# Kernel tuning notes

Measured on AMD Instinct MI355X. Metric: run time of the kernel, lower is better.

## Reference

```python
import jax, jax.numpy as jnp
import numpy as np

B, N, DIM = 2, 2048, 512
HEADS, DIM_HEAD = 8, 64
INNER = HEADS * DIM_HEAD  # 512
SCALE = DIM_HEAD ** -0.5


def setup_inputs() -> dict:
    key = jax.random.key(0)
    k1, k2, k3, k4, k5 = jax.random.split(key, 5)
    s = 0.02
    return {
        "x1": jax.random.normal(k1, (B, N, DIM), jnp.float32),
        "x2": jax.random.normal(k2, (B, N, DIM), jnp.float32),
        "W_qk": jax.random.normal(k3, (DIM, 2 * INNER), jnp.float32) * s,
        "W_v": jax.random.normal(k4, (DIM, INNER), jnp.float32) * s,
        "W_out": jax.random.normal(k5, (INNER, DIM), jnp.float32) * s,
        "b_out": jnp.zeros((DIM,), jnp.float32),
    }


def _split_heads(t):
    # [b, n, h*d] -> [b, h, n, d]
    b, n, _ = t.shape
    return t.reshape(b, n, HEADS, DIM_HEAD).transpose(0, 2, 1, 3)


def reference(x1, x2, W_qk, W_v, W_out, b_out):
    # to_qk(x1) -> chunk into k, v ; to_v(x2) -> q  (names in orig are swapped)
    kv = x1 @ W_qk                      # [b, n1, 2*inner]
    k, v = jnp.split(kv, 2, axis=-1)
    q = x2 @ W_v                        # [b, n2, inner]
    q, k, v = _split_heads(q), _split_heads(k), _split_heads(v)  # [b,h,n,d]
    dots = jnp.einsum("bhid,bhjd->bhij", q, k) * SCALE  # [b,h,n2,n1]
    attn = jax.nn.softmax(dots, axis=-1)
    out = jnp.einsum("bhij,bhjd->bhid", attn, v)         # [b,h,n2,d]
    out = out.transpose(0, 2, 1, 3).reshape(out.shape[0], out.shape[2], INNER)
    return out @ W_out + b_out          # [b, n2, dim]
```

## Files before the change

kernel.cpp:

```cpp
#include <hip/hip_runtime.h>

typedef short bf16x8 __attribute__((ext_vector_type(8)));
typedef short bf16x4 __attribute__((ext_vector_type(4)));
typedef float f32x4 __attribute__((ext_vector_type(4)));
typedef float f32x16 __attribute__((ext_vector_type(16)));
typedef unsigned short u16;
typedef unsigned int u32;
typedef u16 u16x8 __attribute__((ext_vector_type(8)));
typedef u16 u16x4 __attribute__((ext_vector_type(4)));

#define DEV __device__ __forceinline__

DEV u16 f2bf(float f) {
  unsigned u = __float_as_uint(f);
  u += 0x7fff + ((u >> 16) & 1);
  return (u16)(u >> 16);
}

DEV int cvtpk(float lo, float hi) {
  int r;
  asm("v_cvt_pk_bf16_f32 %0, %1, %2" : "=v"(r) : "v"(lo), "v"(hi));
  return r;
}

DEV int pkbf(float lo, float hi) {
  return __builtin_amdgcn_perm(__float_as_uint(hi) + 0x8000u,
                               __float_as_uint(lo) + 0x8000u, 0x07060302u);
}

#define MFMA16(a, b, c) __builtin_amdgcn_mfma_f32_16x16x32_bf16(a, b, c, 0, 0, 0)
#define MFMA3216(a, b, c) __builtin_amdgcn_mfma_f32_32x32x16_bf16(a, b, c, 0, 0, 0)

#if __has_builtin(__builtin_amdgcn_mfma_f32_32x32x8bf16_1k)
#define HAVE_PV8 1
#define PVMFMA(a, b, c) __builtin_amdgcn_mfma_f32_32x32x8bf16_1k(a, b, c, 0, 0, 0)
#else
#define HAVE_PV8 0
#endif

#if __has_builtin(__builtin_amdgcn_exp2f)
#define QSCALE 0.18033688011112042f
#define EXPFN(x) __builtin_amdgcn_exp2f(x)
#else
#define QSCALE 0.125f
#define EXPFN(x) __expf(x)
#endif

#define GLD16(gp, lp)                                                     \
  __builtin_amdgcn_global_load_lds(                                       \
      (const __attribute__((address_space(1))) u32*)(gp),                 \
      (__attribute__((address_space(3))) u32*)(lp), 16, 0, 0)

__global__ __launch_bounds__(256) void wprep(
    const float* __restrict__ Wqk, const float* __restrict__ Wv,
    const float* __restrict__ Wout,
    const float* __restrict__ x1, const float* __restrict__ x2,
    u16* __restrict__ WqkT, u16* __restrict__ WvT, u16* __restrict__ WoutT,
    u16* __restrict__ x1b, u16* __restrict__ x2b) {
  __shared__ float tf[32][33];
  int bx = blockIdx.x, t = threadIdx.x;
  if (bx >= 1024) {
    int id = bx - 1024;
    const float* src = id < 1024 ? x1 : x2;
    u16* dst = id < 1024 ? x1b : x2b;
    long base = (long)(id & 1023) * 2048 + t * 8;
    float4 f0 = *(const float4*)(src + base);
    float4 f1 = *(const float4*)(src + base + 4);
    u16x8 o;
    o[0] = f2bf(f0.x); o[1] = f2bf(f0.y); o[2] = f2bf(f0.z); o[3] = f2bf(f0.w);
    o[4] = f2bf(f1.x); o[5] = f2bf(f1.y); o[6] = f2bf(f1.z); o[7] = f2bf(f1.w);
    *(u16x8*)(dst + base) = o;
    return;
  }
  const float* src; u16* dst; int Ncols; int id;
  if (bx < 512)      { id = bx;       src = Wqk;  dst = WqkT;  Ncols = 1024; }
  else if (bx < 768) { id = bx - 512; src = Wv;   dst = WvT;   Ncols = 512; }
  else               { id = bx - 768; src = Wout; dst = WoutT; Ncols = 512; }
  int tilesPerRow = Ncols >> 5;
  int tr = id / tilesPerRow, tc = id % tilesPerRow;
  int r0 = tr * 32, c0 = tc * 32;
  {
    int r = t >> 3, c4 = (t & 7) * 4;
    float4 v = *(const float4*)(src + (long)(r0 + r) * Ncols + c0 + c4);
    tf[r][c4] = v.x; tf[r][c4 + 1] = v.y; tf[r][c4 + 2] = v.z; tf[r][c4 + 3] = v.w;
  }
  __syncthreads();
  {
    int c = t >> 3, r4 = (t & 7) * 4;
    u16x4 o;
    o[0] = f2bf(tf[r4][c]); o[1] = f2bf(tf[r4 + 1][c]);
    o[2] = f2bf(tf[r4 + 2][c]); o[3] = f2bf(tf[r4 + 3][c]);
    *(u16x4*)(dst + (long)(c0 + c) * 512 + r0 + r4) = o;
  }
}

__global__ __launch_bounds__(256) void qkv_gemm(
    const u16* __restrict__ x1b, const u16* __restrict__ x2b,
    const u16* __restrict__ WqkT, const u16* __restrict__ WvT,
    u16* __restrict__ out_q, u16* __restrict__ out_k, u16* __restrict__ out_vt) {
  __shared__ u16 sA[2][128 * 40];
  __shared__ u16 sB[2][64 * 40];
  int bx = blockIdx.x, t = threadIdx.x;
  bool isQ = bx < 256;
  int bx2 = isQ ? bx : bx - 256;
  const u16* Ap = isQ ? x2b : x1b;
  const u16* BT = isQ ? WvT : WqkT;
  int m0 = (bx2 & 31) * 128, n0 = (bx2 >> 5) * 64;
  int w = t >> 6, l = t & 63, lm = l & 15, lq = l >> 4;

  f32x4 zero = {0.f, 0.f, 0.f, 0.f};
  f32x4 acc[2][4];
#pragma unroll
  for (int i = 0; i < 2; ++i)
#pragma unroll
    for (int j = 0; j < 4; ++j) acc[i][j] = zero;

  int sm = t >> 2;
  int skc = (t & 3) * 8;
  const u16* gA = Ap + (long)(m0 + sm) * 512 + skc;
  const u16* gB = BT + (long)(n0 + sm) * 512 + skc;

  bf16x8 a0 = *(const bf16x8*)(gA);
  bf16x8 a1 = *(const bf16x8*)(gA + 64 * 512);
  bf16x8 b0 = *(const bf16x8*)(gB);
  *(bf16x8*)(sA[0] + sm * 40 + skc) = a0;
  *(bf16x8*)(sA[0] + (sm + 64) * 40 + skc) = a1;
  *(bf16x8*)(sB[0] + sm * 40 + skc) = b0;
  __syncthreads();

  for (int kt = 0; kt < 16; ++kt) {
    int cur = kt & 1;
    if (kt < 15) {
      a0 = *(const bf16x8*)(gA + (kt + 1) * 32);
      a1 = *(const bf16x8*)(gA + 64 * 512 + (kt + 1) * 32);
      b0 = *(const bf16x8*)(gB + (kt + 1) * 32);
    }
    bf16x8 af[2], bfr[4];
    af[0] = *(const bf16x8*)(sA[cur] + (w * 32 + lm) * 40 + lq * 8);
    af[1] = *(const bf16x8*)(sA[cur] + (w * 32 + 16 + lm) * 40 + lq * 8);
#pragma unroll
    for (int s = 0; s < 4; ++s)
      bfr[s] = *(const bf16x8*)(sB[cur] + (s * 16 + lm) * 40 + lq * 8);
#pragma unroll
    for (int ms = 0; ms < 2; ++ms)
#pragma unroll
      for (int s = 0; s < 4; ++s)
        acc[ms][s] = MFMA16(af[ms], bfr[s], acc[ms][s]);
    if (kt < 15) {
      int nxt = 1 - cur;
      *(bf16x8*)(sA[nxt] + sm * 40 + skc) = a0;
      *(bf16x8*)(sA[nxt] + (sm + 64) * 40 + skc) = a1;
      *(bf16x8*)(sB[nxt] + sm * 40 + skc) = b0;
    }
    __syncthreads();
  }

#pragma unroll
  for (int ms = 0; ms < 2; ++ms) {
    int gmBase = m0 + w * 32 + ms * 16 + lq * 4;
#pragma unroll
    for (int s = 0; s < 4; ++s) {
      int gc = n0 + s * 16 + lm;
      int b = gmBase >> 11, n = gmBase & 2047;
      if (isQ) {
#pragma unroll
        for (int r = 0; r < 4; ++r)
          out_q[(((long)(b << 3) + (gc >> 6)) * 2048 + n + r) * 64 + (gc & 63)] =
              f2bf(acc[ms][s][r] * QSCALE);
      } else if (gc < 512) {
#pragma unroll
        for (int r = 0; r < 4; ++r)
          out_k[(((long)(b << 3) + (gc >> 6)) * 2048 + n + r) * 64 + (gc & 63)] =
              f2bf(acc[ms][s][r]);
      } else {
        int c = gc - 512, h = c >> 6, d = c & 63;
        u16x4 vv;
#pragma unroll
        for (int r = 0; r < 4; ++r) vv[r] = f2bf(acc[ms][s][r]);
        *(u16x4*)(out_vt + (((long)(b << 3) + h) * 64 + d) * 2048 + n) = vv;
      }
    }
  }
}

__global__ __launch_bounds__(256, 2) void attn(
    const u16* __restrict__ Q, const u16* __restrict__ K,
    const u16* __restrict__ Vt, u16* __restrict__ O) {
  int id = blockIdx.x;
  int bh = id & 15, qt = id >> 4;
  int b = bh >> 3, h = bh & 7;
  const u16* Kh = K + (long)bh * 2048 * 64;
  const u16* Vh = Vt + (long)bh * 64 * 2048;
  int t = threadIdx.x, w = t >> 6, lane = t & 63, ln = lane & 31, hi = lane >> 5;
  int g = w & 1, kh = w >> 1;

  __shared__ u16 smem[2][2][2][4096];

  bf16x8 qf[4];
  {
    const u16* qp = Q + (long)bh * 2048 * 64 + (long)(qt * 64 + g * 32 + ln) * 64 + hi * 8;
#pragma unroll
    for (int dc = 0; dc < 4; ++dc) qf[dc] = *(const bf16x8*)(qp + dc * 16);
  }

  f32x16 accO[2];
#pragma unroll
  for (int dt = 0; dt < 2; ++dt)
#pragma unroll
    for (int i = 0; i < 16; ++i) accO[dt][i] = 0.f;
  float dacc = 0.f;

  f32x16 fz;
#pragma unroll
  for (int i = 0; i < 16; ++i) fz[i] = 0.f;

  int lrow = lane >> 3;
  int swz = ((lane & 7) ^ lrow) * 8;
  const u16* gKl = Kh + (long)(kh * 1024 + g * 32 + lrow) * 64 + swz;
  const u16* gVl = Vh + (long)(g * 32 + lrow) * 2048 + kh * 1024 + swz;

  auto stage = [&](int jt, int buf) {
    u16* sK = smem[buf][0][kh];
    u16* sV = smem[buf][1][kh];
    const u16* gk = gKl + (long)jt * 4096;
    const u16* gv = gVl + jt * 64;
#pragma unroll
    for (int i = 0; i < 4; ++i) {
      GLD16(gk + i * 512, sK + (g * 32 + i * 8) * 64);
      GLD16(gv + (long)i * 16384, sV + (g * 32 + i * 8) * 64);
    }
  };

  stage(0, 0);
  __syncthreads();

  int swl = ln & 7;
  for (int jt = 0; jt < 16; ++jt) {
    int cur = jt & 1;
    if (jt < 15) stage(jt + 1, cur ^ 1);
    const u16* sKh = smem[cur][0][kh];
    const u16* sVh = smem[cur][1][kh];
#pragma unroll
    for (int kt2 = 0; kt2 < 2; ++kt2) {
      int rowK = (kt2 * 32 + ln) * 64;
      bf16x8 kf0 = *(const bf16x8*)(sKh + rowK + ((0 * 2 + hi) ^ swl) * 8);
      bf16x8 kf1 = *(const bf16x8*)(sKh + rowK + ((1 * 2 + hi) ^ swl) * 8);
      bf16x8 kf2 = *(const bf16x8*)(sKh + rowK + ((2 * 2 + hi) ^ swl) * 8);
      bf16x8 kf3 = *(const bf16x8*)(sKh + rowK + ((3 * 2 + hi) ^ swl) * 8);
      __builtin_amdgcn_s_setprio(1);
      f32x16 st = MFMA3216(kf0, qf[0], fz);
      st = MFMA3216(kf1, qf[1], st);
      st = MFMA3216(kf2, qf[2], st);
      st = MFMA3216(kf3, qf[3], st);
      __builtin_amdgcn_s_setprio(0);
      float p[16];
#pragma unroll
      for (int i = 0; i < 16; ++i) p[i] = EXPFN(st[i]);
      float q0 = (p[0] + p[1]) + (p[2] + p[3]);
      float q1 = (p[4] + p[5]) + (p[6] + p[7]);
      float q2 = (p[8] + p[9]) + (p[10] + p[11]);
      float q3 = (p[12] + p[13]) + (p[14] + p[15]);
      dacc += (q0 + q1) + (q2 + q3);
#if HAVE_PV8
      __builtin_amdgcn_s_setprio(1);
#pragma unroll
      for (int c = 0; c < 4; ++c) {
        union { int2 i2; bf16x4 v; } u;
        u.i2.x = cvtpk(p[c * 4 + 0], p[c * 4 + 1]);
        u.i2.y = cvtpk(p[c * 4 + 2], p[c * 4 + 3]);
#pragma unroll
        for (int dt = 0; dt < 2; ++dt) {
          bf16x4 vf = *(const bf16x4*)(sVh + (dt * 32 + ln) * 64 +
                                       (((kt2 * 4 + c) ^ swl) * 8) + hi * 4);
          accO[dt] = PVMFMA(vf, u.v, accO[dt]);
        }
      }
      __builtin_amdgcn_s_setprio(0);
#else
      __builtin_amdgcn_s_setprio(1);
#pragma unroll
      for (int c2 = 0; c2 < 2; ++c2) {
        int o0x = pkbf(p[c2 * 8 + 0], p[c2 * 8 + 1]);
        int o0y = pkbf(p[c2 * 8 + 2], p[c2 * 8 + 3]);
        int o1x = pkbf(p[c2 * 8 + 4], p[c2 * 8 + 5]);
        int o1y = pkbf(p[c2 * 8 + 6], p[c2 * 8 + 7]);
        int s0x = __shfl_xor(o0x, 32), s0y = __shfl_xor(o0y, 32);
        int s1x = __shfl_xor(o1x, 32), s1y = __shfl_xor(o1y, 32);
        union { int4 i4; bf16x8 v; } u;
        if (hi) { u.i4.x = s1x; u.i4.y = s1y; u.i4.z = o1x; u.i4.w = o1y; }
        else    { u.i4.x = o0x; u.i4.y = o0y; u.i4.z = s0x; u.i4.w = s0y; }
#pragma unroll
        for (int dt = 0; dt < 2; ++dt) {
          bf16x8 vf = *(const bf16x8*)(sVh + (dt * 32 + ln) * 64 +
                                       (((kt2 * 4 + c2 * 2 + hi) ^ swl) * 8));
          accO[dt] = MFMA3216(vf, u.v, accO[dt]);
        }
      }
      __builtin_amdgcn_s_setprio(0);
#endif
    }
    __syncthreads();
  }

  float* cb = (float*)&smem[0][0][0][0];
  float* base = cb + g * 2112;
  if (kh == 1) {
#pragma unroll
    for (int dt = 0; dt < 2; ++dt)
#pragma unroll
      for (int i = 0; i < 16; ++i)
        base[(dt * 16 + i) * 64 + hi * 32 + ln] = accO[dt][i];
    base[2048 + hi * 32 + ln] = dacc;
  }
  __syncthreads();
  if (kh == 0) {
#pragma unroll
    for (int dt = 0; dt < 2; ++dt)
#pragma unroll
      for (int i = 0; i < 16; ++i)
        accO[dt][i] += base[(dt * 16 + i) * 64 + hi * 32 + ln];
    dacc += base[2048 + hi * 32 + ln];
    dacc += __shfl_xor(dacc, 32);
    float inv = 1.f / dacc;

    u16* Ob = O + ((long)b * 2048 + qt * 64 + g * 32 + ln) * 512 + h * 64;
#pragma unroll
    for (int dt = 0; dt < 2; ++dt)
#pragma unroll
      for (int gq = 0; gq < 4; ++gq) {
        u16x4 o;
#pragma unroll
        for (int rr = 0; rr < 4; ++rr) o[rr] = f2bf(accO[dt][gq * 4 + rr] * inv);
        *(u16x4*)(Ob + dt * 32 + gq * 8 + hi * 4) = o;
      }
  }
}

__global__ __launch_bounds__(128) void out_gemm(
    const u16* __restrict__ A, const u16* __restrict__ BT,
    float* __restrict__ out_f, const float* __restrict__ bias) {
  __shared__ u16 sA[2][64 * 40];
  __shared__ u16 sB[2][32 * 40];
  int t = threadIdx.x, bx = blockIdx.x;
  int m0 = (bx & 63) * 64, n0 = (bx >> 6) * 32;
  int w = t >> 6, l = t & 63, lm = l & 15, lq = l >> 4;

  f32x4 zero = {0.f, 0.f, 0.f, 0.f};
  f32x4 acc[2][2];
#pragma unroll
  for (int i = 0; i < 2; ++i)
#pragma unroll
    for (int j = 0; j < 2; ++j) acc[i][j] = zero;

  int ar = t >> 1, akc = (t & 1) * 16;
  int br = t >> 2, bkc = (t & 3) * 8;
  const u16* gA = A + (long)(m0 + ar) * 512 + akc;
  const u16* gB = BT + (long)(n0 + br) * 512 + bkc;

  bf16x8 a0 = *(const bf16x8*)(gA);
  bf16x8 a1 = *(const bf16x8*)(gA + 8);
  bf16x8 b0 = *(const bf16x8*)(gB);
  *(bf16x8*)(sA[0] + ar * 40 + akc) = a0;
  *(bf16x8*)(sA[0] + ar * 40 + akc + 8) = a1;
  *(bf16x8*)(sB[0] + br * 40 + bkc) = b0;
  __syncthreads();

  for (int kt = 0; kt < 16; ++kt) {
    int cur = kt & 1;
    if (kt < 15) {
      a0 = *(const bf16x8*)(gA + (kt + 1) * 32);
      a1 = *(const bf16x8*)(gA + (kt + 1) * 32 + 8);
      b0 = *(const bf16x8*)(gB + (kt + 1) * 32);
    }
    bf16x8 af[2], bfr[2];
    af[0] = *(const bf16x8*)(sA[cur] + (w * 32 + lm) * 40 + lq * 8);
    af[1] = *(const bf16x8*)(sA[cur] + (w * 32 + 16 + lm) * 40 + lq * 8);
    bfr[0] = *(const bf16x8*)(sB[cur] + (lm)*40 + lq * 8);
    bfr[1] = *(const bf16x8*)(sB[cur] + (16 + lm) * 40 + lq * 8);
#pragma unroll
    for (int ms = 0; ms < 2; ++ms)
#pragma unroll
      for (int s = 0; s < 2; ++s)
        acc[ms][s] = MFMA16(af[ms], bfr[s], acc[ms][s]);
    if (kt < 15) {
      int nxt = 1 - cur;
      *(bf16x8*)(sA[nxt] + ar * 40 + akc) = a0;
      *(bf16x8*)(sA[nxt] + ar * 40 + akc + 8) = a1;
      *(bf16x8*)(sB[nxt] + br * 40 + bkc) = b0;
    }
    __syncthreads();
  }

#pragma unroll
  for (int ms = 0; ms < 2; ++ms) {
    int gmBase = m0 + w * 32 + ms * 16 + lq * 4;
#pragma unroll
    for (int s = 0; s < 2; ++s) {
      int gc = n0 + s * 16 + lm;
      float bv = bias[gc];
#pragma unroll
      for (int r = 0; r < 4; ++r)
        out_f[(long)(gmBase + r) * 512 + gc] = acc[ms][s][r] + bv;
    }
  }
}

extern "C" void kernel_launch(void* const* d_in, const int* in_sizes, int n_in,
                              void* d_out, int out_size, void* d_ws, size_t ws_size,
                              hipStream_t stream) {
  const float* x1 = (const float*)d_in[0];
  const float* x2 = (const float*)d_in[1];
  const float* Wqk = (const float*)d_in[2];
  const float* Wv = (const float*)d_in[3];
  const float* Wout = (const float*)d_in[4];
  const float* bout = (const float*)d_in[5];
  float* out = (float*)d_out;

  u16* ws = (u16*)d_ws;
  const long SZ = 2097152;
  u16* Qw = ws;
  u16* Kw = ws + SZ;
  u16* Vtw = ws + 2 * SZ;
  u16* Ow = ws + 3 * SZ;
  u16* WqkT = ws + 4 * SZ;
  u16* WvT = WqkT + 524288;
  u16* WoutT = WvT + 262144;
  u16* x1b = WoutT + 262144;
  u16* x2b = x1b + SZ;

  wprep<<<3072, 256, 0, stream>>>(Wqk, Wv, Wout, x1, x2, WqkT, WvT, WoutT, x1b, x2b);
  qkv_gemm<<<768, 256, 0, stream>>>(x1b, x2b, WqkT, WvT, Qw, Kw, Vtw);
  attn<<<512, 256, 0, stream>>>(Qw, Kw, Vtw, Ow);
  out_gemm<<<1024, 128, 0, stream>>>(Ow, WoutT, out, bout);
}
```

Before: 127.4 us.

## Fuse fp32-to-bf16 activation conversion into QKV GEMM via direct-to-LDS loads

Drops the separate pass that converted x1/x2 to bf16 in the prep kernel. The QKV GEMM now streams fp32 activations straight into an XOR-swizzled LDS tile with global_load_lds and converts them to bf16 on the fly with packed cvt instructions before the MFMA. This removes a full write and re-read of the bf16 activation copies and shrinks the prep launch. In exchange the GEMM reads twice the bytes per A tile and spends extra ALU work converting values, and A-tile LDS use doubles.

```diff
diff --git a/kernel.cpp b/kernel.cpp
--- a/kernel.cpp
+++ b/kernel.cpp
@@ -54,24 +54,9 @@
 __global__ __launch_bounds__(256) void wprep(
     const float* __restrict__ Wqk, const float* __restrict__ Wv,
     const float* __restrict__ Wout,
-    const float* __restrict__ x1, const float* __restrict__ x2,
-    u16* __restrict__ WqkT, u16* __restrict__ WvT, u16* __restrict__ WoutT,
-    u16* __restrict__ x1b, u16* __restrict__ x2b) {
+    u16* __restrict__ WqkT, u16* __restrict__ WvT, u16* __restrict__ WoutT) {
   __shared__ float tf[32][33];
   int bx = blockIdx.x, t = threadIdx.x;
-  if (bx >= 1024) {
-    int id = bx - 1024;
-    const float* src = id < 1024 ? x1 : x2;
-    u16* dst = id < 1024 ? x1b : x2b;
-    long base = (long)(id & 1023) * 2048 + t * 8;
-    float4 f0 = *(const float4*)(src + base);
-    float4 f1 = *(const float4*)(src + base + 4);
-    u16x8 o;
-    o[0] = f2bf(f0.x); o[1] = f2bf(f0.y); o[2] = f2bf(f0.z); o[3] = f2bf(f0.w);
-    o[4] = f2bf(f1.x); o[5] = f2bf(f1.y); o[6] = f2bf(f1.z); o[7] = f2bf(f1.w);
-    *(u16x8*)(dst + base) = o;
-    return;
-  }
   const float* src; u16* dst; int Ncols; int id;
   if (bx < 512)      { id = bx;       src = Wqk;  dst = WqkT;  Ncols = 1024; }
   else if (bx < 768) { id = bx - 512; src = Wv;   dst = WvT;   Ncols = 512; }
@@ -95,15 +80,15 @@
 }
 
 __global__ __launch_bounds__(256) void qkv_gemm(
-    const u16* __restrict__ x1b, const u16* __restrict__ x2b,
+    const float* __restrict__ x1, const float* __restrict__ x2,
     const u16* __restrict__ WqkT, const u16* __restrict__ WvT,
     u16* __restrict__ out_q, u16* __restrict__ out_k, u16* __restrict__ out_vt) {
-  __shared__ u16 sA[2][128 * 40];
-  __shared__ u16 sB[2][64 * 40];
+  __shared__ __align__(16) float sA32[2][128 * 32];
+  __shared__ __align__(16) u16 sB[2][64 * 40];
   int bx = blockIdx.x, t = threadIdx.x;
   bool isQ = bx < 256;
   int bx2 = isQ ? bx : bx - 256;
-  const u16* Ap = isQ ? x2b : x1b;
+  const float* Ap = isQ ? x2 : x1;
   const u16* BT = isQ ? WvT : WqkT;
   int m0 = (bx2 & 31) * 128, n0 = (bx2 >> 5) * 64;
   int w = t >> 6, l = t & 63, lm = l & 15, lq = l >> 4;
@@ -115,29 +100,45 @@
 #pragma unroll
     for (int j = 0; j < 4; ++j) acc[i][j] = zero;
 
+  int dr = l >> 3;
+  int dc = (l & 7) ^ dr;
+  const float* gAsrc = Ap + (long)(m0 + w * 32 + dr) * 512 + dc * 4;
+
+  auto stageA = [&](int kt, int buf) {
+#pragma unroll
+    for (int i = 0; i < 4; ++i)
+      GLD16(gAsrc + kt * 32 + i * 8 * 512, sA32[buf] + (w * 32 + i * 8) * 32);
+  };
+
   int sm = t >> 2;
   int skc = (t & 3) * 8;
-  const u16* gA = Ap + (long)(m0 + sm) * 512 + skc;
   const u16* gB = BT + (long)(n0 + sm) * 512 + skc;
 
-  bf16x8 a0 = *(const bf16x8*)(gA);
-  bf16x8 a1 = *(const bf16x8*)(gA + 64 * 512);
+  stageA(0, 0);
   bf16x8 b0 = *(const bf16x8*)(gB);
-  *(bf16x8*)(sA[0] + sm * 40 + skc) = a0;
-  *(bf16x8*)(sA[0] + (sm + 64) * 40 + skc) = a1;
   *(bf16x8*)(sB[0] + sm * 40 + skc) = b0;
   __syncthreads();
 
+  int sw7 = lm & 7;
   for (int kt = 0; kt < 16; ++kt) {
     int cur = kt & 1;
     if (kt < 15) {
-      a0 = *(const bf16x8*)(gA + (kt + 1) * 32);
-      a1 = *(const bf16x8*)(gA + 64 * 512 + (kt + 1) * 32);
+      stageA(kt + 1, cur ^ 1);
       b0 = *(const bf16x8*)(gB + (kt + 1) * 32);
     }
     bf16x8 af[2], bfr[4];
-    af[0] = *(const bf16x8*)(sA[cur] + (w * 32 + lm) * 40 + lq * 8);
-    af[1] = *(const bf16x8*)(sA[cur] + (w * 32 + 16 + lm) * 40 + lq * 8);
+#pragma unroll
+    for (int ms = 0; ms < 2; ++ms) {
+      const float* rp = sA32[cur] + (w * 32 + ms * 16 + lm) * 32;
+      f32x4 c0 = *(const f32x4*)(rp + ((2 * lq) ^ sw7) * 4);
+      f32x4 c1 = *(const f32x4*)(rp + ((2 * lq + 1) ^ sw7) * 4);
+      union { int4 i; bf16x8 v; } ua;
+      ua.i.x = cvtpk(c0[0], c0[1]);
+      ua.i.y = cvtpk(c0[2], c0[3]);
+      ua.i.z = cvtpk(c1[0], c1[1]);
+      ua.i.w = cvtpk(c1[2], c1[3]);
+      af[ms] = ua.v;
+    }
 #pragma unroll
     for (int s = 0; s < 4; ++s)
       bfr[s] = *(const bf16x8*)(sB[cur] + (s * 16 + lm) * 40 + lq * 8);
@@ -146,12 +147,8 @@
 #pragma unroll
       for (int s = 0; s < 4; ++s)
         acc[ms][s] = MFMA16(af[ms], bfr[s], acc[ms][s]);
-    if (kt < 15) {
-      int nxt = 1 - cur;
-      *(bf16x8*)(sA[nxt] + sm * 40 + skc) = a0;
-      *(bf16x8*)(sA[nxt] + (sm + 64) * 40 + skc) = a1;
-      *(bf16x8*)(sB[nxt] + sm * 40 + skc) = b0;
-    }
+    if (kt < 15)
+      *(bf16x8*)(sB[cur ^ 1] + sm * 40 + skc) = b0;
     __syncthreads();
   }
 
@@ -425,11 +422,9 @@
   u16* WqkT = ws + 4 * SZ;
   u16* WvT = WqkT + 524288;
   u16* WoutT = WvT + 262144;
-  u16* x1b = WoutT + 262144;
-  u16* x2b = x1b + SZ;
-
-  wprep<<<3072, 256, 0, stream>>>(Wqk, Wv, Wout, x1, x2, WqkT, WvT, WoutT, x1b, x2b);
-  qkv_gemm<<<768, 256, 0, stream>>>(x1b, x2b, WqkT, WvT, Qw, Kw, Vtw);
+
+  wprep<<<1024, 256, 0, stream>>>(Wqk, Wv, Wout, WqkT, WvT, WoutT);
+  qkv_gemm<<<768, 256, 0, stream>>>(x1, x2, WqkT, WvT, Qw, Kw, Vtw);
   attn<<<512, 256, 0, stream>>>(Qw, Kw, Vtw, Ow);
   out_gemm<<<1024, 128, 0, stream>>>(Ow, WoutT, out, bout);
 }
```

New measurement: 126.8 us, median of 2. No clear change (-0.4%).
